# Optimization experiments

Measured on AMD Instinct MI355X. Metric: run time of the kernel, lower is better.

Reference implementation:

```python
import jax, jax.numpy as jnp
import numpy as np

STATE_DIM = 32
ACTION_DIM = 8
LATENT_DIM = 64
HIDDEN = 128
X_DIM = ACTION_DIM + 1  # t channel + actions
B = 4096
L = 128
N_SUB = 2  # fixed RK4 substeps per knot interval


def natural_cubic_coeffs(x):
    """Natural cubic spline on unit-spaced knots 0..L-1 (matches torchcde's
    implicit arange grid). x: [B, L, C]. Returns per-interval coeffs b, c, d
    ([B, L-1, C]) s.t. X(i+u) = x_i + b u + c u^2 + d u^3."""
    Bb, Ln, C = x.shape
    n = Ln - 2
    # tridiagonal system for interior second derivatives (natural BC: m0=mL-1=0)
    M = 4.0 * jnp.eye(n, dtype=x.dtype) + jnp.eye(n, k=1, dtype=x.dtype) + jnp.eye(n, k=-1, dtype=x.dtype)
    rhs = 6.0 * (x[:, 2:] - 2.0 * x[:, 1:-1] + x[:, :-2])  # [B, n, C]
    m_in = jnp.linalg.solve(M, rhs.transpose(1, 0, 2).reshape(n, -1))  # [n, B*C]
    m_in = m_in.reshape(n, Bb, C).transpose(1, 0, 2)
    zpad = jnp.zeros((Bb, 1, C), x.dtype)
    m = jnp.concatenate([zpad, m_in, zpad], axis=1)  # [B, L, C]
    b = (x[:, 1:] - x[:, :-1]) - (2.0 * m[:, :-1] + m[:, 1:]) / 6.0
    c = m[:, :-1] / 2.0
    d = (m[:, 1:] - m[:, :-1]) / 6.0
    return b, c, d


def setup_inputs() -> dict:
    key = jax.random.key(0)
    ks = jax.random.split(key, 8)
    s = jax.random.normal(ks[0], (B, L, STATE_DIM), dtype=jnp.float32)
    a = jax.random.normal(ks[1], (B, L, ACTION_DIM), dtype=jnp.float32)
    t = jnp.broadcast_to(jnp.arange(L, dtype=jnp.float32), (B, L)) + jnp.zeros((B, L), jnp.float32)

    def lin(k, fi, fo, scale=1.0):
        return (jax.random.normal(k, (fi, fo), dtype=jnp.float32) * (scale / np.sqrt(fi))).astype(jnp.float32)

    enc_W = lin(ks[2], STATE_DIM + ACTION_DIM + 1, LATENT_DIM)
    enc_b = jnp.zeros((LATENT_DIM,), jnp.float32)
    f_W1 = lin(ks[3], LATENT_DIM, HIDDEN, 0.5)
    f_b1 = jnp.zeros((HIDDEN,), jnp.float32)
    f_W2 = lin(ks[4], HIDDEN, LATENT_DIM * X_DIM, 0.1)  # small scale keeps the CDE stable over 127 time units
    f_b2 = jnp.zeros((LATENT_DIM * X_DIM,), jnp.float32)
    dec_W = lin(ks[5], LATENT_DIM, STATE_DIM)
    dec_b = jnp.zeros((STATE_DIM,), jnp.float32)
    return dict(s=s, a=a, t=t, enc_W=enc_W, enc_b=enc_b, f_W1=f_W1, f_b1=f_b1,
                f_W2=f_W2, f_b2=f_b2, dec_W=dec_W, dec_b=dec_b)


def reference(s, a, t, enc_W, enc_b, f_W1, f_b1, f_W2, f_b2, dec_W, dec_b):
    # control path X = [t, a] : [B, L, X_DIM]
    x = jnp.concatenate([t[..., None], a], axis=-1)
    cb, cc, cd = natural_cubic_coeffs(x)  # each [B, L-1, X_DIM]

    z0 = jnp.concatenate([s[:, 0], a[:, 0], t[:, 0:1]], axis=-1) @ enc_W + enc_b  # [B, latent]

    def vf(z):  # f(z): [B, latent] -> [B, latent, X_DIM]
        h = jax.nn.relu(z @ f_W1 + f_b1)
        return (h @ f_W2 + f_b2).reshape(-1, LATENT_DIM, X_DIM)

    hstep = 1.0 / N_SUB

    def interval(z, coef):
        bi, ci, di = coef  # [B, X_DIM] each, current interval spline coeffs

        def dzdu(z, u):
            dX = bi + 2.0 * ci * u + 3.0 * di * (u * u)  # dX/dt on this interval
            return jnp.einsum('blx,bx->bl', vf(z), dX)

        for k in range(N_SUB):  # small fixed unroll, not a data-dim loop
            u = k * hstep
            k1 = dzdu(z, u)
            k2 = dzdu(z + 0.5 * hstep * k1, u + 0.5 * hstep)
            k3 = dzdu(z + 0.5 * hstep * k2, u + 0.5 * hstep)
            k4 = dzdu(z + hstep * k3, u + hstep)
            z = z + (hstep / 6.0) * (k1 + 2.0 * k2 + 2.0 * k3 + k4)
        return z, z

    coefs = (cb.transpose(1, 0, 2), cc.transpose(1, 0, 2), cd.transpose(1, 0, 2))  # [L-1, B, X_DIM]
    _, zs = jax.lax.scan(interval, z0, coefs)  # zs: [L-1, B, latent]
    z = jnp.concatenate([z0[None], zs], axis=0).transpose(1, 0, 2)  # [B, L, latent]
    return z @ dec_W + dec_b  # [B, L, state_dim]
```

## Files before the change

kernel.cpp:

```cpp
#include <hip/hip_runtime.h>

#define Bsz 4096
#define Lsz 128
#define NI  127
#define SD  32
#define AD  8
#define LAT 64
#define HID 128
#define BT  16
#define THR 512

typedef float f32x2 __attribute__((ext_vector_type(2)));
typedef float f32x4 __attribute__((ext_vector_type(4)));

__global__ __launch_bounds__(256) void repack_w2(const float* __restrict__ W2,
                                                 float* __restrict__ W2p8,
                                                 float* __restrict__ W2c0){
  int idx = blockIdx.x*256 + threadIdx.x;
  if (idx < HID*LAT*8){
    int x = idx & 7; int jl = idx >> 3; int l = jl & 63; int j = jl >> 6;
    W2p8[idx] = W2[(j*LAT + l)*9 + x + 1];
  } else if (idx < HID*LAT*9){
    int jl = idx - HID*LAT*8;
    W2c0[jl] = W2[(size_t)jl*9];
  }
}

__global__ __launch_bounds__(256) void spline_kernel(const float* __restrict__ a,
                                                     float* __restrict__ m_ws){
  __shared__ float cp_s[126];
  if (threadIdx.x == 0){
    float c = 0.25f; cp_s[0] = c;
    for (int i=1;i<126;i++){ c = 1.0f/(4.0f - c); cp_s[i] = c; }
  }
  __syncthreads();
  int tid = blockIdx.x*256 + threadIdx.x;
  int b = tid >> 3, c8 = tid & 7;
  float dp[126];
  const float* ab = a + (size_t)b*Lsz*AD + c8;
  float x0 = ab[0];
  float x1 = ab[AD];
  for (int i=0;i<126;i++){
    float x2 = ab[(size_t)(i+2)*AD];
    float rhs = 6.0f*(x2 - 2.0f*x1 + x0);
    dp[i] = (i==0)? rhs*0.25f : (rhs - dp[i-1])*cp_s[i];
    x0 = x1; x1 = x2;
  }
  m_ws[tid] = 0.0f;
  m_ws[((size_t)127*Bsz)*8 + tid] = 0.0f;
  float mn = 0.0f;
  for (int k=125;k>=0;k--){
    mn = dp[k] - cp_s[k]*mn;
    m_ws[((size_t)(k+1)*Bsz)*8 + tid] = mn;
  }
}

#define DPP_XOR1(v) __int_as_float(__builtin_amdgcn_mov_dpp(__float_as_int(v), 0xB1, 0xF, 0xF, true))
#define DPP_XOR2(v) __int_as_float(__builtin_amdgcn_mov_dpp(__float_as_int(v), 0x4E, 0xF, 0xF, true))
#define SWZ_XOR4(v) __int_as_float(__builtin_amdgcn_ds_swizzle(__float_as_int(v), 0x101F))

#define PK_MUL_BCLO(d, w, x) asm("v_pk_mul_f32 %0, %1, %2 op_sel:[0,0] op_sel_hi:[0,1]" : "=v"(d) : "v"(w), "v"(x))
#define PK_MUL_BCHI(d, w, x) asm("v_pk_mul_f32 %0, %1, %2 op_sel:[1,0] op_sel_hi:[1,1]" : "=v"(d) : "v"(w), "v"(x))
#define PK_FMA_BCLO(acc, w, x) asm("v_pk_fma_f32 %0, %1, %2, %0 op_sel:[0,0,0] op_sel_hi:[0,1,1]" : "+v"(acc) : "v"(w), "v"(x))
#define PK_FMA_BCHI(acc, w, x) asm("v_pk_fma_f32 %0, %1, %2, %0 op_sel:[1,0,0] op_sel_hi:[1,1,1]" : "+v"(acc) : "v"(w), "v"(x))
#define PK_FMA(acc, a, b)      asm("v_pk_fma_f32 %0, %1, %2, %0" : "+v"(acc) : "v"(a), "v"(b))
#define PK_ADD(d, a, b)        asm("v_pk_add_f32 %0, %1, %2" : "=v"(d) : "v"(a), "v"(b))

#define LO2(v4) __builtin_shufflevector(v4, v4, 0, 1)
#define HI2(v4) __builtin_shufflevector(v4, v4, 2, 3)

__attribute__((amdgpu_waves_per_eu(2,2)))
__global__ __launch_bounds__(THR) void cde_integrate(
    const float* __restrict__ s, const float* __restrict__ a, const float* __restrict__ t,
    const float* __restrict__ encW, const float* __restrict__ encb,
    const float* __restrict__ W1, const float* __restrict__ b1,
    const float* __restrict__ b2, const float* __restrict__ decW, const float* __restrict__ decb,
    const float* __restrict__ W2p8, const float* __restrict__ W2c0, const float* __restrict__ m_ws,
    float* __restrict__ out)
{
  __shared__ float W1t[HID][LAT+4];
  __shared__ float hp[8][292];
  __shared__ float zp[8][132];
  __shared__ float dXp[5][8][20];
  __shared__ float dWs[LAT][SD];
  __shared__ float dbs[SD];

  const int tid = threadIdx.x;
  const int b0 = blockIdx.x * BT;
  const int ol = tid >> 3;
  const int jg = tid & 7;

  for (int i=tid;i<HID*LAT;i+=THR){ int j = i & (HID-1); int k = i >> 7; W1t[j][k] = W1[k*HID+j]; }
  for (int i=tid;i<LAT*SD;i+=THR)  ((float*)dWs)[i] = decW[i];
  if (tid < SD) dbs[tid] = decb[tid];

  f32x2 wpk[16][4]; f32x2 wc0pk[8];
  {
    #pragma unroll
    for (int jj=0;jj<16;jj++){
      const f32x2* p2 = (const f32x2*)&W2p8[((size_t)(jg*16+jj)*LAT + ol)*8];
      wpk[jj][0]=p2[0]; wpk[jj][1]=p2[1]; wpk[jj][2]=p2[2]; wpk[jj][3]=p2[3];
    }
    #pragma unroll
    for (int q=0;q<8;q++){
      wc0pk[q].x = W2c0[(jg*16+2*q)*LAT + ol];
      wc0pk[q].y = W2c0[(jg*16+2*q+1)*LAT + ol];
    }
  }
  f32x2 b2p[4]; f32x2 b2c0v; f32x2 b1pair; f32x2 one11; one11.x = 1.f; one11.y = 1.f;
  {
    const float* bp = b2 + ol*9;
    b2c0v.x = bp[0]; b2c0v.y = 0.f;
    b2p[0].x = bp[1]; b2p[0].y = bp[2];
    b2p[1].x = bp[3]; b2p[1].y = bp[4];
    b2p[2].x = bp[5]; b2p[2].y = bp[6];
    b2p[3].x = bp[7]; b2p[3].y = bp[8];
    b1pair.x = b1[2*ol]; b1pair.y = b1[2*ol+1];
  }

  {
    const int bb8 = tid >> 6;
    const int li = tid & 63;
    #pragma unroll
    for (int h=0; h<2; h++){
      const int b = bb8 + 8*h;
      const float* sb = s + (size_t)(b0+b)*Lsz*SD;
      const float* ab = a + (size_t)(b0+b)*Lsz*AD;
      const float tv = t[(size_t)(b0+b)*Lsz];
      float acc = encb[li];
      #pragma unroll
      for (int k=0;k<SD;k++) acc = fmaf(sb[k], encW[k*LAT+li], acc);
      #pragma unroll
      for (int k=0;k<AD;k++) acc = fmaf(ab[k], encW[(SD+k)*LAT+li], acc);
      acc = fmaf(tv, encW[(SD+AD)*LAT+li], acc);
      zp[b>>1][li*2 + (b&1)] = acc;
    }
  }
  __syncthreads();

  {
    const int bb = tid >> 5; const int o = tid & 31; const int c = bb & 1;
    const float* zrow = &zp[bb>>1][0];
    float acc = dbs[o];
    #pragma unroll 16
    for (int k=0;k<LAT;k++) acc = fmaf(zrow[2*k+c], dWs[k][o], acc);
    out[((size_t)(b0+bb)*Lsz + 0)*SD + o] = acc;
  }

  float zb0, zb1, ka0 = 0.f, ka1 = 0.f;
  { f32x2 zr = *(const f32x2*)&zp[jg][2*ol]; zb0 = zr.x; zb1 = zr.y; }

  #pragma unroll 1
  for (int iv=0; iv<NI; iv++){
    for (int idx=tid; idx<5*BT*8; idx+=THR){
      int ui = idx >> 7; int r = idx & 127; int bb = r >> 3; int x8 = r & 7;
      float u = 0.25f*(float)ui;
      int gb = b0+bb;
      float m0 = m_ws[((size_t)iv    *Bsz + gb)*8 + x8];
      float m1 = m_ws[((size_t)(iv+1)*Bsz + gb)*8 + x8];
      float xd = a[((size_t)gb*Lsz + iv+1)*AD + x8] - a[((size_t)gb*Lsz + iv)*AD + x8];
      float cb = xd - (2.f*m0 + m1)*(1.f/6.f);
      float cc = 0.5f*m0;
      float cd = (m1 - m0)*(1.f/6.f);
      dXp[ui][bb>>1][x8*2 + (bb&1)] = cb + (2.f*cc)*u + (3.f*cd)*(u*u);
    }

    #pragma unroll 1
    for (int st=0; st<8; st++){
      const int ui = (st+1)>>1;
      const int mode = st & 3;
      __syncthreads();

      {
        const int j0 = 2*ol;
        f32x2 acc0, acc1;
        PK_MUL_BCLO(acc0, b1pair, one11);
        PK_MUL_BCHI(acc1, b1pair, one11);
        const f32x4* zrow = (const f32x4*)&zp[jg][0];
        const f32x4* w0r = (const f32x4*)&W1t[j0][0];
        const f32x4* w1r = (const f32x4*)&W1t[j0+1][0];
        #pragma unroll
        for (int k16=0;k16<16;k16++){
          f32x4 zqA = zrow[2*k16], zqB = zrow[2*k16+1];
          f32x4 w0q = w0r[k16], w1q = w1r[k16];
          f32x2 w0l = LO2(w0q), w0h = HI2(w0q), w1l = LO2(w1q), w1h = HI2(w1q);
          f32x2 zA0 = LO2(zqA), zA1 = HI2(zqA), zB0 = LO2(zqB), zB1 = HI2(zqB);
          PK_FMA_BCLO(acc0, w0l, zA0); PK_FMA_BCHI(acc0, w0l, zA1);
          PK_FMA_BCLO(acc0, w0h, zB0); PK_FMA_BCHI(acc0, w0h, zB1);
          PK_FMA_BCLO(acc1, w1l, zA0); PK_FMA_BCHI(acc1, w1l, zA1);
          PK_FMA_BCLO(acc1, w1h, zB0); PK_FMA_BCHI(acc1, w1h, zB1);
        }
        f32x4 hv;
        hv.x = fmaxf(acc0.x, 0.f); hv.y = fmaxf(acc0.y, 0.f);
        hv.z = fmaxf(acc1.x, 0.f); hv.w = fmaxf(acc1.y, 0.f);
        *(f32x4*)&hp[jg][(ol>>3)*36 + (ol&7)*4] = hv;
      }
      __syncthreads();

      f32x2 dz[8];
      #pragma unroll
      for (int p=0;p<8;p++){ dz[p].x = 0.f; dz[p].y = 0.f; }
      #pragma unroll
      for (int ch=0; ch<2; ch++){
        f32x2 cw[8][4]; f32x2 cc4[4];
        #pragma unroll
        for (int q=0;q<8;q++){
          cw[q][0]=wpk[ch*8+q][0]; cw[q][1]=wpk[ch*8+q][1];
          cw[q][2]=wpk[ch*8+q][2]; cw[q][3]=wpk[ch*8+q][3];
          asm volatile("" : "+v"(cw[q][0]), "+v"(cw[q][1]), "+v"(cw[q][2]), "+v"(cw[q][3]));
        }
        #pragma unroll
        for (int q=0;q<4;q++){ cc4[q] = wc0pk[ch*4+q]; }
        asm volatile("" : "+v"(cc4[0]), "+v"(cc4[1]), "+v"(cc4[2]), "+v"(cc4[3]));
        #pragma unroll
        for (int p=0;p<8;p++){
          const f32x4* dxr = (const f32x4*)&dXp[ui][p][0];
          f32x4 d0=dxr[0], d1=dxr[1], d2=dxr[2], d3=dxr[3];
          f32x2 dx2[8] = {LO2(d0),HI2(d0),LO2(d1),HI2(d1),LO2(d2),HI2(d2),LO2(d3),HI2(d3)};
          const f32x4* hr = (const f32x4*)&hp[p][jg*36];
          #pragma unroll
          for (int q2=0;q2<4;q2++){
            f32x4 hq = hr[ch*4 + q2];
            f32x2 hl = LO2(hq), hh = HI2(hq);
            const int ja = 2*q2, jb = 2*q2+1;
            {
              f32x2 wd;
              PK_MUL_BCLO(wd, cw[ja][0], dx2[0]); PK_FMA_BCHI(wd, cw[ja][0], dx2[1]);
              PK_FMA_BCLO(wd, cw[ja][1], dx2[2]); PK_FMA_BCHI(wd, cw[ja][1], dx2[3]);
              PK_FMA_BCLO(wd, cw[ja][2], dx2[4]); PK_FMA_BCHI(wd, cw[ja][2], dx2[5]);
              PK_FMA_BCLO(wd, cw[ja][3], dx2[6]); PK_FMA_BCHI(wd, cw[ja][3], dx2[7]);
              PK_FMA_BCLO(wd, cc4[q2], one11);
              PK_FMA(dz[p], hl, wd);
            }
            {
              f32x2 wd;
              PK_MUL_BCLO(wd, cw[jb][0], dx2[0]); PK_FMA_BCHI(wd, cw[jb][0], dx2[1]);
              PK_FMA_BCLO(wd, cw[jb][1], dx2[2]); PK_FMA_BCHI(wd, cw[jb][1], dx2[3]);
              PK_FMA_BCLO(wd, cw[jb][2], dx2[4]); PK_FMA_BCHI(wd, cw[jb][2], dx2[5]);
              PK_FMA_BCLO(wd, cw[jb][3], dx2[6]); PK_FMA_BCHI(wd, cw[jb][3], dx2[7]);
              PK_FMA_BCHI(wd, cc4[q2], one11);
              PK_FMA(dz[p], hh, wd);
            }
          }
        }
      }

      const bool g1 = jg & 1;
      f32x2 n4[4];
      #pragma unroll
      for (int i=0;i<4;i++){
        f32x2 lo = dz[2*i], hi = dz[2*i+1];
        f32x2 send = g1 ? lo : hi;
        f32x2 recv; recv.x = DPP_XOR1(send.x); recv.y = DPP_XOR1(send.y);
        f32x2 keep = g1 ? hi : lo;
        PK_ADD(n4[i], keep, recv);
      }
      const bool g2 = jg & 2;
      f32x2 n2[2];
      #pragma unroll
      for (int i=0;i<2;i++){
        f32x2 lo = n4[2*i], hi = n4[2*i+1];
        f32x2 send = g2 ? lo : hi;
        f32x2 recv; recv.x = DPP_XOR2(send.x); recv.y = DPP_XOR2(send.y);
        f32x2 keep = g2 ? hi : lo;
        PK_ADD(n2[i], keep, recv);
      }
      const bool g4 = jg & 4;
      f32x2 res;
      {
        f32x2 lo = n2[0], hi = n2[1];
        f32x2 send = g4 ? lo : hi;
        f32x2 recv; recv.x = SWZ_XOR4(send.x); recv.y = SWZ_XOR4(send.y);
        f32x2 keep = g4 ? hi : lo;
        PK_ADD(res, keep, recv);
      }

      f32x2 bias2;
      {
        const f32x4* dxb = (const f32x4*)&dXp[ui][jg][0];
        f32x4 e0=dxb[0], e1=dxb[1], e2=dxb[2], e3=dxb[3];
        PK_MUL_BCLO(bias2, b2c0v, one11);
        PK_FMA_BCLO(bias2, b2p[0], LO2(e0)); PK_FMA_BCHI(bias2, b2p[0], HI2(e0));
        PK_FMA_BCLO(bias2, b2p[1], LO2(e1)); PK_FMA_BCHI(bias2, b2p[1], HI2(e1));
        PK_FMA_BCLO(bias2, b2p[2], LO2(e2)); PK_FMA_BCHI(bias2, b2p[2], HI2(e2));
        PK_FMA_BCLO(bias2, b2p[3], LO2(e3)); PK_FMA_BCHI(bias2, b2p[3], HI2(e3));
      }
      f32x2 dzm2; PK_ADD(dzm2, res, bias2);
      const float dz0 = dzm2.x, dz1 = dzm2.y;

      float zn0, zn1;
      if (mode == 0){
        ka0 = dz0; ka1 = dz1;
        zn0 = fmaf(0.25f, dz0, zb0); zn1 = fmaf(0.25f, dz1, zb1);
      } else if (mode == 1){
        ka0 = fmaf(2.f, dz0, ka0); ka1 = fmaf(2.f, dz1, ka1);
        zn0 = fmaf(0.25f, dz0, zb0); zn1 = fmaf(0.25f, dz1, zb1);
      } else if (mode == 2){
        ka0 = fmaf(2.f, dz0, ka0); ka1 = fmaf(2.f, dz1, ka1);
        zn0 = fmaf(0.5f, dz0, zb0); zn1 = fmaf(0.5f, dz1, zb1);
      } else {
        ka0 += dz0; ka1 += dz1;
        zb0 = fmaf(0.5f/6.f, ka0, zb0); zb1 = fmaf(0.5f/6.f, ka1, zb1);
        zn0 = zb0; zn1 = zb1;
      }
      f32x2 zw; zw.x = zn0; zw.y = zn1;
      *(f32x2*)&zp[jg][2*ol] = zw;
    }

    __syncthreads();
    {
      const int bb = tid >> 5; const int o = tid & 31; const int c = bb & 1;
      const float* zrow = &zp[bb>>1][0];
      float acc = dbs[o];
      #pragma unroll 16
      for (int k=0;k<LAT;k++) acc = fmaf(zrow[2*k+c], dWs[k][o], acc);
      out[((size_t)(b0+bb)*Lsz + (iv+1))*SD + o] = acc;
    }
  }
}

extern "C" void kernel_launch(void* const* d_in, const int* in_sizes, int n_in,
                              void* d_out, int out_size, void* d_ws, size_t ws_size,
                              hipStream_t stream){
  const float* s    = (const float*)d_in[0];
  const float* a    = (const float*)d_in[1];
  const float* t    = (const float*)d_in[2];
  const float* encW = (const float*)d_in[3];
  const float* encb = (const float*)d_in[4];
  const float* W1   = (const float*)d_in[5];
  const float* b1   = (const float*)d_in[6];
  const float* W2   = (const float*)d_in[7];
  const float* b2   = (const float*)d_in[8];
  const float* decW = (const float*)d_in[9];
  const float* decb = (const float*)d_in[10];
  float* out = (float*)d_out;
  float* ws  = (float*)d_ws;
  float* W2p8 = ws;
  float* W2c0 = ws + HID*LAT*8;
  float* m_ws = ws + HID*LAT*9;

  hipLaunchKernelGGL(repack_w2, dim3((HID*LAT*9+255)/256), dim3(256), 0, stream, W2, W2p8, W2c0);
  hipLaunchKernelGGL(spline_kernel, dim3(Bsz*8/256), dim3(256), 0, stream, a, m_ws);
  hipLaunchKernelGGL(cde_integrate, dim3(Bsz/BT), dim3(THR), 0, stream,
                     s,a,t,encW,encb,W1,b1,b2,decW,decb,W2p8,W2c0,m_ws,out);
}
```

Baseline: 9.683 ms.

## Pin W2 weights in AGPRs and split batch reduction into two halves

The packed W2 weight registers are forced into accumulation registers (AGPRs) through inline asm constraints, which frees architectural VGPRs. The per-row dz accumulation is split into two batches of four rows, each reduced on its own with DPP/swizzle exchanges, and each lane keeps the half matching its group. This cuts live dz registers from 8 pairs to 4, which lowers VGPR pressure and may avoid spills. The cost is extra AGPR-to-VGPR copies each chunk, the weight chunks being reloaded twice per step, and a full xor4 reduction in each batch that does redundant work.

```diff
diff --git a/kernel.cpp b/kernel.cpp
--- a/kernel.cpp
+++ b/kernel.cpp
@@ -106,6 +106,12 @@
       wc0pk[q].x = W2c0[(jg*16+2*q)*LAT + ol];
       wc0pk[q].y = W2c0[(jg*16+2*q+1)*LAT + ol];
     }
+    #pragma unroll
+    for (int jj=0;jj<16;jj++){
+      asm volatile("" : "+a"(wpk[jj][0]), "+a"(wpk[jj][1]), "+a"(wpk[jj][2]), "+a"(wpk[jj][3]));
+    }
+    asm volatile("" : "+a"(wc0pk[0]), "+a"(wc0pk[1]), "+a"(wc0pk[2]), "+a"(wc0pk[3]),
+                      "+a"(wc0pk[4]), "+a"(wc0pk[5]), "+a"(wc0pk[6]), "+a"(wc0pk[7]));
   }
   f32x2 b2p[4]; f32x2 b2c0v; f32x2 b1pair; f32x2 one11; one11.x = 1.f; one11.y = 1.f;
   {
@@ -197,82 +203,85 @@
       }
       __syncthreads();
 
-      f32x2 dz[8];
+      f32x2 resKeep; resKeep.x = 0.f; resKeep.y = 0.f;
       #pragma unroll
-      for (int p=0;p<8;p++){ dz[p].x = 0.f; dz[p].y = 0.f; }
-      #pragma unroll
-      for (int ch=0; ch<2; ch++){
-        f32x2 cw[8][4]; f32x2 cc4[4];
+      for (int bbat=0; bbat<2; bbat++){
+        f32x2 dz[4];
         #pragma unroll
-        for (int q=0;q<8;q++){
-          cw[q][0]=wpk[ch*8+q][0]; cw[q][1]=wpk[ch*8+q][1];
-          cw[q][2]=wpk[ch*8+q][2]; cw[q][3]=wpk[ch*8+q][3];
-          asm volatile("" : "+v"(cw[q][0]), "+v"(cw[q][1]), "+v"(cw[q][2]), "+v"(cw[q][3]));
-        }
+        for (int i=0;i<4;i++){ dz[i].x = 0.f; dz[i].y = 0.f; }
         #pragma unroll
-        for (int q=0;q<4;q++){ cc4[q] = wc0pk[ch*4+q]; }
-        asm volatile("" : "+v"(cc4[0]), "+v"(cc4[1]), "+v"(cc4[2]), "+v"(cc4[3]));
-        #pragma unroll
-        for (int p=0;p<8;p++){
-          const f32x4* dxr = (const f32x4*)&dXp[ui][p][0];
-          f32x4 d0=dxr[0], d1=dxr[1], d2=dxr[2], d3=dxr[3];
-          f32x2 dx2[8] = {LO2(d0),HI2(d0),LO2(d1),HI2(d1),LO2(d2),HI2(d2),LO2(d3),HI2(d3)};
-          const f32x4* hr = (const f32x4*)&hp[p][jg*36];
+        for (int ch=0; ch<2; ch++){
+          f32x2 cw[8][4]; f32x2 cc[4];
           #pragma unroll
-          for (int q2=0;q2<4;q2++){
-            f32x4 hq = hr[ch*4 + q2];
-            f32x2 hl = LO2(hq), hh = HI2(hq);
-            const int ja = 2*q2, jb = 2*q2+1;
-            {
-              f32x2 wd;
-              PK_MUL_BCLO(wd, cw[ja][0], dx2[0]); PK_FMA_BCHI(wd, cw[ja][0], dx2[1]);
-              PK_FMA_BCLO(wd, cw[ja][1], dx2[2]); PK_FMA_BCHI(wd, cw[ja][1], dx2[3]);
-              PK_FMA_BCLO(wd, cw[ja][2], dx2[4]); PK_FMA_BCHI(wd, cw[ja][2], dx2[5]);
-              PK_FMA_BCLO(wd, cw[ja][3], dx2[6]); PK_FMA_BCHI(wd, cw[ja][3], dx2[7]);
-              PK_FMA_BCLO(wd, cc4[q2], one11);
-              PK_FMA(dz[p], hl, wd);
-            }
-            {
-              f32x2 wd;
-              PK_MUL_BCLO(wd, cw[jb][0], dx2[0]); PK_FMA_BCHI(wd, cw[jb][0], dx2[1]);
-              PK_FMA_BCLO(wd, cw[jb][1], dx2[2]); PK_FMA_BCHI(wd, cw[jb][1], dx2[3]);
-              PK_FMA_BCLO(wd, cw[jb][2], dx2[4]); PK_FMA_BCHI(wd, cw[jb][2], dx2[5]);
-              PK_FMA_BCLO(wd, cw[jb][3], dx2[6]); PK_FMA_BCHI(wd, cw[jb][3], dx2[7]);
-              PK_FMA_BCHI(wd, cc4[q2], one11);
-              PK_FMA(dz[p], hh, wd);
+          for (int q=0;q<8;q++){
+            cw[q][0]=wpk[ch*8+q][0]; cw[q][1]=wpk[ch*8+q][1];
+            cw[q][2]=wpk[ch*8+q][2]; cw[q][3]=wpk[ch*8+q][3];
+          }
+          #pragma unroll
+          for (int q=0;q<4;q++) cc[q]=wc0pk[ch*4+q];
+          #pragma unroll
+          for (int q=0;q<8;q++){
+            asm volatile("" : "+v"(cw[q][0]), "+v"(cw[q][1]), "+v"(cw[q][2]), "+v"(cw[q][3]));
+          }
+          asm volatile("" : "+v"(cc[0]), "+v"(cc[1]), "+v"(cc[2]), "+v"(cc[3]));
+          #pragma unroll
+          for (int pi=0; pi<4; pi++){
+            const int p = bbat*4 + pi;
+            const f32x4* dxr = (const f32x4*)&dXp[ui][p][0];
+            f32x4 d0=dxr[0], d1=dxr[1], d2=dxr[2], d3=dxr[3];
+            f32x2 dx2[8] = {LO2(d0),HI2(d0),LO2(d1),HI2(d1),LO2(d2),HI2(d2),LO2(d3),HI2(d3)};
+            const f32x4* hr = (const f32x4*)&hp[p][jg*36 + ch*16];
+            #pragma unroll
+            for (int q2=0;q2<4;q2++){
+              f32x4 hq = hr[q2];
+              f32x2 hl = LO2(hq), hh = HI2(hq);
+              const int ja = 2*q2, jb = 2*q2+1;
+              {
+                f32x2 wd;
+                PK_MUL_BCLO(wd, cw[ja][0], dx2[0]); PK_FMA_BCHI(wd, cw[ja][0], dx2[1]);
+                PK_FMA_BCLO(wd, cw[ja][1], dx2[2]); PK_FMA_BCHI(wd, cw[ja][1], dx2[3]);
+                PK_FMA_BCLO(wd, cw[ja][2], dx2[4]); PK_FMA_BCHI(wd, cw[ja][2], dx2[5]);
+                PK_FMA_BCLO(wd, cw[ja][3], dx2[6]); PK_FMA_BCHI(wd, cw[ja][3], dx2[7]);
+                PK_FMA_BCLO(wd, cc[q2], one11);
+                PK_FMA(dz[pi], hl, wd);
+              }
+              {
+                f32x2 wd;
+                PK_MUL_BCLO(wd, cw[jb][0], dx2[0]); PK_FMA_BCHI(wd, cw[jb][0], dx2[1]);
+                PK_FMA_BCLO(wd, cw[jb][1], dx2[2]); PK_FMA_BCHI(wd, cw[jb][1], dx2[3]);
+                PK_FMA_BCLO(wd, cw[jb][2], dx2[4]); PK_FMA_BCHI(wd, cw[jb][2], dx2[5]);
+                PK_FMA_BCLO(wd, cw[jb][3], dx2[6]); PK_FMA_BCHI(wd, cw[jb][3], dx2[7]);
+                PK_FMA_BCHI(wd, cc[q2], one11);
+                PK_FMA(dz[pi], hh, wd);
+              }
             }
           }
         }
-      }
-
-      const bool g1 = jg & 1;
-      f32x2 n4[4];
-      #pragma unroll
-      for (int i=0;i<4;i++){
-        f32x2 lo = dz[2*i], hi = dz[2*i+1];
-        f32x2 send = g1 ? lo : hi;
-        f32x2 recv; recv.x = DPP_XOR1(send.x); recv.y = DPP_XOR1(send.y);
-        f32x2 keep = g1 ? hi : lo;
-        PK_ADD(n4[i], keep, recv);
-      }
-      const bool g2 = jg & 2;
-      f32x2 n2[2];
-      #pragma unroll
-      for (int i=0;i<2;i++){
-        f32x2 lo = n4[2*i], hi = n4[2*i+1];
-        f32x2 send = g2 ? lo : hi;
-        f32x2 recv; recv.x = DPP_XOR2(send.x); recv.y = DPP_XOR2(send.y);
-        f32x2 keep = g2 ? hi : lo;
-        PK_ADD(n2[i], keep, recv);
-      }
-      const bool g4 = jg & 4;
-      f32x2 res;
-      {
-        f32x2 lo = n2[0], hi = n2[1];
-        f32x2 send = g4 ? lo : hi;
-        f32x2 recv; recv.x = SWZ_XOR4(send.x); recv.y = SWZ_XOR4(send.y);
-        f32x2 keep = g4 ? hi : lo;
-        PK_ADD(res, keep, recv);
+        const bool g1 = jg & 1;
+        f32x2 n2[2];
+        #pragma unroll
+        for (int i=0;i<2;i++){
+          f32x2 lo = dz[2*i], hi = dz[2*i+1];
+          f32x2 send = g1 ? lo : hi;
+          f32x2 recv; recv.x = DPP_XOR1(send.x); recv.y = DPP_XOR1(send.y);
+          f32x2 keep = g1 ? hi : lo;
+          PK_ADD(n2[i], keep, recv);
+        }
+        const bool g2 = jg & 2;
+        f32x2 n1;
+        {
+          f32x2 lo = n2[0], hi = n2[1];
+          f32x2 send = g2 ? lo : hi;
+          f32x2 recv; recv.x = DPP_XOR2(send.x); recv.y = DPP_XOR2(send.y);
+          f32x2 keep = g2 ? hi : lo;
+          PK_ADD(n1, keep, recv);
+        }
+        f32x2 res;
+        {
+          f32x2 recv; recv.x = SWZ_XOR4(n1.x); recv.y = SWZ_XOR4(n1.y);
+          PK_ADD(res, n1, recv);
+        }
+        if ((jg>>2) == bbat) resKeep = res;
       }
 
       f32x2 bias2;
@@ -285,7 +294,7 @@
         PK_FMA_BCLO(bias2, b2p[2], LO2(e2)); PK_FMA_BCHI(bias2, b2p[2], HI2(e2));
         PK_FMA_BCLO(bias2, b2p[3], LO2(e3)); PK_FMA_BCHI(bias2, b2p[3], HI2(e3));
       }
-      f32x2 dzm2; PK_ADD(dzm2, res, bias2);
+      f32x2 dzm2; PK_ADD(dzm2, resKeep, bias2);
       const float dz0 = dzm2.x, dz1 = dzm2.y;
 
       float zn0, zn1;
```

New measurement: 19.41 ms. 2x slower.
